# Performance work log

Hardware: AMD Instinct MI355X
Metric: run time of the kernel (lower is better)

Reference implementation:

```python
import jax, jax.numpy as jnp
import numpy as np

DIM = 256
NUM_HEADS = 4
HEAD_DIM = DIM // NUM_HEADS


def _linear_params(k, d_in, d_out):
    kw, kb = jax.random.split(k)
    lim = 1.0 / np.sqrt(d_in)
    W = jax.random.uniform(kw, (d_out, d_in), jnp.float32, -lim, lim)
    b = jax.random.uniform(kb, (d_out,), jnp.float32, -lim, lim)
    return W, b


def setup_inputs() -> dict:
    key = jax.random.key(0)
    ks = jax.random.split(key, 10)
    B, Nq, Nkv = 8, 4096, 256
    inp = {
        'node_emb': jax.random.normal(ks[0], (B, Nq, DIM), jnp.float32),
        'cluster_emb': jax.random.normal(ks[1], (B, Nkv, DIM), jnp.float32),
        'clustering_weights': jax.random.normal(ks[2], (B, Nq, Nkv), jnp.float32),
        'ln_q_g': jnp.ones((DIM,), jnp.float32), 'ln_q_b': jnp.zeros((DIM,), jnp.float32),
        'ln_kv_g': jnp.ones((DIM,), jnp.float32), 'ln_kv_b': jnp.zeros((DIM,), jnp.float32),
        'ln_out_g': jnp.ones((DIM,), jnp.float32), 'ln_out_b': jnp.zeros((DIM,), jnp.float32),
    }
    for name, k in [('q', ks[3]), ('k', ks[4]), ('v', ks[5]), ('o', ks[6])]:
        W, b = _linear_params(k, DIM, DIM)
        inp[f'W_{name}'], inp[f'b_{name}'] = W, b
    W1, b1 = _linear_params(ks[7], DIM, DIM)
    W2, b2 = _linear_params(ks[8], DIM, DIM)
    inp.update(W_m1=W1, b_m1=b1, W_m2=W2, b_m2=b2)
    return inp


def _layer_norm(x, g, b, eps=1e-5):
    mu = jnp.mean(x, axis=-1, keepdims=True)
    var = jnp.var(x, axis=-1, keepdims=True)
    return (x - mu) * jax.lax.rsqrt(var + eps) * g + b


def reference(node_emb, cluster_emb, clustering_weights,
              ln_q_g, ln_q_b, ln_kv_g, ln_kv_b, ln_out_g, ln_out_b,
              W_q, b_q, W_k, b_k, W_v, b_v, W_o, b_o,
              W_m1, b_m1, W_m2, b_m2):
    B, Nq, D = node_emb.shape
    Nkv = cluster_emb.shape[1]
    q_in = _layer_norm(node_emb, ln_q_g, ln_q_b)
    kv_in = _layer_norm(cluster_emb, ln_kv_g, ln_kv_b)
    # projections -> [B, H, N, hd]
    Q = (q_in @ W_q.T + b_q).reshape(B, Nq, NUM_HEADS, HEAD_DIM).transpose(0, 2, 1, 3)
    K = (kv_in @ W_k.T + b_k).reshape(B, Nkv, NUM_HEADS, HEAD_DIM).transpose(0, 2, 1, 3)
    V = (kv_in @ W_v.T + b_v).reshape(B, Nkv, NUM_HEADS, HEAD_DIM).transpose(0, 2, 1, 3)
    scores = jnp.einsum('bhqd,bhkd->bhqk', Q, K) / np.sqrt(HEAD_DIM)
    scores = scores + clustering_weights[:, None, :, :]
    attn = jax.nn.softmax(scores, axis=-1)
    ctx = jnp.einsum('bhqk,bhkd->bhqd', attn, V)
    ctx = ctx.transpose(0, 2, 1, 3).reshape(B, Nq, D)
    attn_out = ctx @ W_o.T + b_o
    x = node_emb + attn_out
    h = _layer_norm(x, ln_out_g, ln_out_b)
    h = jax.nn.gelu(h @ W_m1.T + b_m1, approximate=False) @ W_m2.T + b_m2
    out = x + h
    attn_matrix = attn.mean(axis=1)
    return out, attn_matrix
```

## Files before the change

### kernel.cpp

```cpp
#include <hip/hip_runtime.h>
#include <math.h>

typedef __attribute__((ext_vector_type(8))) short short8;
typedef __attribute__((ext_vector_type(4))) float f32x4;
typedef __attribute__((ext_vector_type(2))) unsigned int u32x2;

#define AS1 __attribute__((address_space(1)))
#define AS3 __attribute__((address_space(3)))

__device__ __forceinline__ float b2f(short s){
  return __uint_as_float(((unsigned int)(unsigned short)s) << 16);
}
__device__ __forceinline__ short f2b(float f){
  unsigned int u = __float_as_uint(f);
  u = (u + 0x7fffu + ((u >> 16) & 1u)) >> 16;
  return (short)u;
}
__device__ __forceinline__ unsigned pk2(float lo, float hi){
  return ((unsigned)(unsigned short)f2b(hi) << 16) | (unsigned)(unsigned short)f2b(lo);
}

__global__ __launch_bounds__(256) void cvt_w(
    const float* __restrict__ s0, const float* __restrict__ s1,
    const float* __restrict__ s2, const float* __restrict__ s3,
    const float* __restrict__ s4, const float* __restrict__ s5,
    short* __restrict__ dst)
{
  const float* srcs[6] = {s0, s1, s2, s3, s4, s5};
  int i = blockIdx.x * 256 + threadIdx.x;
  dst[i] = f2b(srcs[i >> 16][i & 65535]);
}

__global__ __launch_bounds__(256) void ln_k(
    const float* __restrict__ x, const float* __restrict__ g,
    const float* __restrict__ bta, short* __restrict__ y)
{
  const int row = blockIdx.x, t = threadIdx.x;
  const size_t base = (size_t)row * 256;
  float v = x[base + t];
  float s1 = v, s2 = v * v;
  #pragma unroll
  for (int off = 32; off; off >>= 1){ s1 += __shfl_down(s1, off); s2 += __shfl_down(s2, off); }
  __shared__ float a1[4], a2[4];
  __shared__ float mu_s, rs_s;
  if ((t & 63) == 0){ a1[t >> 6] = s1; a2[t >> 6] = s2; }
  __syncthreads();
  if (t == 0){
    float S1 = a1[0] + a1[1] + a1[2] + a1[3];
    float S2 = a2[0] + a2[1] + a2[2] + a2[3];
    float mu = S1 * 0.00390625f;
    float var = S2 * 0.00390625f - mu * mu;
    mu_s = mu; rs_s = rsqrtf(var + 1e-5f);
  }
  __syncthreads();
  y[base + t] = f2b((v - mu_s) * rs_s * g[t] + bta[t]);
}

template<int OT, int LNA>
__global__ __launch_bounds__(256, 2) void gemmW(
    const short* __restrict__ A, const float* __restrict__ Af,
    const short* __restrict__ W, const float* __restrict__ bias,
    short* __restrict__ outB,
    const float* __restrict__ lnag, const float* __restrict__ lnab)
{
  __shared__ short As[64][264];
  __shared__ short Ws[2][256][40];
  const int tid = threadIdx.x;
  const int m0 = blockIdx.x << 6;
  const int w = tid >> 6, lane = tid & 63;
  const int l15 = lane & 15, g = lane >> 4;

  if (LNA){
    const int row = tid >> 2, c0 = (tid & 3) << 6;
    float vv[64];
    const float* src = &Af[(size_t)(m0 + row) * 256 + c0];
    #pragma unroll
    for (int i = 0; i < 16; ++i) *(f32x4*)&vv[4 * i] = *(const f32x4*)&src[4 * i];
    float s1 = 0.f, s2 = 0.f;
    #pragma unroll
    for (int i = 0; i < 64; ++i){ s1 += vv[i]; s2 += vv[i] * vv[i]; }
    s1 += __shfl_xor(s1, 1); s2 += __shfl_xor(s2, 1);
    s1 += __shfl_xor(s1, 2); s2 += __shfl_xor(s2, 2);
    const float mu = s1 * 0.00390625f;
    const float rs = rsqrtf(s2 * 0.00390625f - mu * mu + 1e-5f);
    #pragma unroll
    for (int i = 0; i < 8; ++i){
      f32x4 gv0 = *(const f32x4*)&lnag[c0 + 8 * i];
      f32x4 gv1 = *(const f32x4*)&lnag[c0 + 8 * i + 4];
      f32x4 bv0 = *(const f32x4*)&lnab[c0 + 8 * i];
      f32x4 bv1 = *(const f32x4*)&lnab[c0 + 8 * i + 4];
      short8 o;
      #pragma unroll
      for (int j = 0; j < 4; ++j) o[j] = f2b((vv[8 * i + j] - mu) * rs * gv0[j] + bv0[j]);
      #pragma unroll
      for (int j = 0; j < 4; ++j) o[4 + j] = f2b((vv[8 * i + 4 + j] - mu) * rs * gv1[j] + bv1[j]);
      *(short8*)&As[row][c0 + 8 * i] = o;
    }
  } else {
    #pragma unroll
    for (int it = 0; it < 8; ++it){
      int idx = tid + (it << 8);
      int row = idx >> 5, c = (idx & 31) << 3;
      *(short8*)&As[row][c] = *(const short8*)&A[(size_t)(m0 + row) * 256 + c];
    }
  }
  #pragma unroll
  for (int it = 0; it < 4; ++it){
    int row = (it << 6) + (tid >> 2), c = (tid & 3) << 3;
    *(short8*)&Ws[0][row][c] = *(const short8*)&W[(size_t)row * 256 + c];
  }
  __syncthreads();

  f32x4 acc[16];
  #pragma unroll
  for (int nt = 0; nt < 16; ++nt) acc[nt] = {0.f, 0.f, 0.f, 0.f};

  int cur = 0;
  for (int s = 0; s < 8; ++s){
    const int k0 = s << 5;
    short8 wreg[4];
    if (s < 7){
      #pragma unroll
      for (int it = 0; it < 4; ++it)
        wreg[it] = *(const short8*)&W[(size_t)((it << 6) + (tid >> 2)) * 256 + k0 + 32 + ((tid & 3) << 3)];
    }
    short8 af = *(const short8*)&As[(w << 4) + l15][k0 + (g << 3)];
    #pragma unroll
    for (int nt = 0; nt < 16; ++nt){
      short8 bf = *(const short8*)&Ws[cur][(nt << 4) + l15][g << 3];
      acc[nt] = __builtin_amdgcn_mfma_f32_16x16x32_bf16(af, bf, acc[nt], 0, 0, 0);
    }
    if (s < 7){
      #pragma unroll
      for (int it = 0; it < 4; ++it)
        *(short8*)&Ws[cur ^ 1][(it << 6) + (tid >> 2)][(tid & 3) << 3] = wreg[it];
    }
    __syncthreads();
    cur ^= 1;
  }

  const int row_l = (w << 4) + (g << 2);
  #pragma unroll
  for (int nt = 0; nt < 16; ++nt){
    const int col = (nt << 4) + l15;
    const float bv = bias[col];
    #pragma unroll
    for (int r = 0; r < 4; ++r){
      const int m = m0 + row_l + r;
      float v = acc[nt][r] + bv;
      if (OT == 1){
        const int b_ = m >> 8, kvr = m & 255;
        const int knt = kvr >> 4, kl = kvr & 15;
        const int h = col >> 6, half = (col >> 5) & 1, kg = (col >> 3) & 3, kj = col & 7;
        outB[(((((size_t)(b_ * 4 + h) * 16 + knt) * 2 + half) * 4 + kg) * 16 + kl) * 8 + kj] = f2b(v);
      }
      if (OT == 2){
        const int b_ = m >> 8, kvj = m & 255;
        const int jp = (kvj & ~31) | (((kvj >> 2) & 3) << 3) | (((kvj >> 4) & 1) << 2) | (kvj & 3);
        const int h = col >> 6, dp = col & 63;
        const int kk = jp >> 5, vg = (jp >> 3) & 3, vj = jp & 7;
        const int vn2 = dp >> 4, vl = dp & 15;
        outB[(((((size_t)(b_ * 4 + h) * 8 + kk) * 4 + vn2) * 4 + vg) * 16 + vl) * 8 + vj] = f2b(v);
      }
      if (OT == 4){
        outB[((((size_t)blockIdx.x * 8 + (col >> 5)) * 4 + w) * 64
              + (((col >> 3) & 3) << 4) + (g << 2) + r) * 8 + (col & 7)] = f2b(v);
      }
    }
  }
}

__global__ __launch_bounds__(256, 2) void attn_k(
    const short* __restrict__ Qf, const short* __restrict__ Kf,
    const short* __restrict__ Vf, const float* __restrict__ cw,
    short* __restrict__ ctx, float* __restrict__ am_out)
{
  extern __shared__ __align__(16) short smem[];
  short* Kl = smem;
  short* Vl = smem + 16384;
  const int b = blockIdx.y;
  const int q0 = blockIdx.x << 6;
  const int tid = threadIdx.x;
  const int w = tid >> 6, lane = tid & 63;
  const int l15 = lane & 15, g = lane >> 4;
  const size_t qw = (size_t)b * 4096 + q0 + (w << 4);
  const size_t qblk = qw >> 4;
  const size_t tileQ = qblk >> 2;
  const int wQ = (int)(qblk & 3);
  const size_t tileC = (size_t)b * 64 + blockIdx.x;

#define STG(dst_, src_) do{ _Pragma("unroll")                                        \
  for (int it_ = 0; it_ < 8; ++it_){ int c_ = (it_ << 8) + tid;                      \
    __builtin_amdgcn_global_load_lds((const AS1 void*)((src_) + (c_ << 3)),          \
                                     (AS3 void*)((dst_) + (c_ << 3)), 16, 0, 0); } }while(0)

  unsigned cwp[16][2];
  f32x4 am[16];
  {
    char* reg = (char*)smem + (w << 13);
    #pragma unroll
    for (int j = 0; j < 16; ++j){
      f32x4 v = *(const f32x4*)&cw[(qw + j) * 256 + (lane << 2)];
      u32x2 d = { pk2(v[0], v[1]), pk2(v[2], v[3]) };
      unsigned off = ((j << 9) + (lane << 3)) ^ ((j & 7) << 4);
      *(u32x2*)(reg + off) = d;
    }
    __syncthreads();
    #pragma unroll
    for (int nt = 0; nt < 16; ++nt){
      unsigned base = ((l15 << 9) + (nt << 5) + (g << 3)) ^ ((l15 & 7) << 4);
      cwp[nt][0] = *(const unsigned*)(reg + base);
      cwp[nt][1] = *(const unsigned*)(reg + base + 4);
      am[nt] = {0.f, 0.f, 0.f, 0.f};
    }
    __syncthreads();
  }

  STG(Kl, Kf + ((size_t)(b * 4) << 14));
  __syncthreads();

  for (int h = 0; h < 4; ++h){
    STG(Vl, Vf + ((size_t)(b * 4 + h) << 14));
    short8 qf0 = *(const short8*)&Qf[(((tileQ * 8 + (h << 1)) * 4 + wQ) * 64 + lane) * 8];
    short8 qf1 = *(const short8*)&Qf[(((tileQ * 8 + (h << 1) + 1) * 4 + wQ) * 64 + lane) * 8];

    f32x4 acc[16];
    #pragma unroll
    for (int nt = 0; nt < 16; ++nt) acc[nt] = {0.f, 0.f, 0.f, 0.f};
    #pragma unroll
    for (int nt = 0; nt < 16; ++nt){
      short8 kf0 = *(const short8*)&Kl[(nt << 10) + (lane << 3)];
      acc[nt] = __builtin_amdgcn_mfma_f32_16x16x32_bf16(kf0, qf0, acc[nt], 0, 0, 0);
      short8 kf1 = *(const short8*)&Kl[(nt << 10) + 512 + (lane << 3)];
      acc[nt] = __builtin_amdgcn_mfma_f32_16x16x32_bf16(kf1, qf1, acc[nt], 0, 0, 0);
    }
    __syncthreads();
    if (h < 3) STG(Kl, Kf + ((size_t)(b * 4 + h + 1) << 14));

    float mx = -3.4e38f;
    #pragma unroll
    for (int nt = 0; nt < 16; ++nt){
      float c0 = __uint_as_float(cwp[nt][0] << 16);
      float c1 = __uint_as_float(cwp[nt][0] & 0xffff0000u);
      float c2 = __uint_as_float(cwp[nt][1] << 16);
      float c3 = __uint_as_float(cwp[nt][1] & 0xffff0000u);
      acc[nt][0] = acc[nt][0] * 0.125f + c0;
      acc[nt][1] = acc[nt][1] * 0.125f + c1;
      acc[nt][2] = acc[nt][2] * 0.125f + c2;
      acc[nt][3] = acc[nt][3] * 0.125f + c3;
      mx = fmaxf(mx, fmaxf(fmaxf(acc[nt][0], acc[nt][1]), fmaxf(acc[nt][2], acc[nt][3])));
    }
    mx = fmaxf(mx, __shfl_xor(mx, 16));
    mx = fmaxf(mx, __shfl_xor(mx, 32));
    float sm = 0.f;
    #pragma unroll
    for (int nt = 0; nt < 16; ++nt){
      #pragma unroll
      for (int r = 0; r < 4; ++r){
        float e = __expf(acc[nt][r] - mx);
        acc[nt][r] = e; sm += e;
      }
    }
    sm += __shfl_xor(sm, 16);
    sm += __shfl_xor(sm, 32);
    float inv = 1.f / sm;
    #pragma unroll
    for (int nt = 0; nt < 16; ++nt){
      #pragma unroll
      for (int r = 0; r < 4; ++r){
        float p = acc[nt][r] * inv;
        acc[nt][r] = p;
        am[nt][r] += 0.25f * p;
      }
    }
    f32x4 oc[4] = {{0,0,0,0},{0,0,0,0},{0,0,0,0},{0,0,0,0}};
    #pragma unroll
    for (int kk = 0; kk < 8; ++kk){
      union { short8 s; unsigned u[4]; } pa;
      pa.u[0] = pk2(acc[2 * kk][0],     acc[2 * kk][1]);
      pa.u[1] = pk2(acc[2 * kk][2],     acc[2 * kk][3]);
      pa.u[2] = pk2(acc[2 * kk + 1][0], acc[2 * kk + 1][1]);
      pa.u[3] = pk2(acc[2 * kk + 1][2], acc[2 * kk + 1][3]);
      #pragma unroll
      for (int n2 = 0; n2 < 4; ++n2){
        short8 vb = *(const short8*)&Vl[(((kk << 2) + n2) << 9) + (lane << 3)];
        oc[n2] = __builtin_amdgcn_mfma_f32_16x16x32_bf16(pa.s, vb, oc[n2], 0, 0, 0);
      }
    }
    #pragma unroll
    for (int n2 = 0; n2 < 4; ++n2){
      const int sctx = (h << 1) + (n2 >> 1);
      const int gctx = ((n2 & 1) << 1) + (l15 >> 3);
      const int j = l15 & 7;
      #pragma unroll
      for (int r = 0; r < 4; ++r)
        ctx[(((tileC * 8 + sctx) * 4 + w) * 64 + (gctx << 4) + (g << 2) + r) * 8 + j]
            = f2b(oc[n2][r]);
    }
    __syncthreads();
  }

  {
    char* reg = (char*)smem + (w << 14);
    #pragma unroll
    for (int nt = 0; nt < 16; ++nt){
      unsigned off = ((l15 << 10) + (nt << 6) + (g << 4)) ^ ((l15 & 7) << 4);
      *(f32x4*)(reg + off) = am[nt];
    }
    __syncthreads();
    #pragma unroll
    for (int i2 = 0; i2 < 16; ++i2){
      unsigned fb = (tid << 4) + (i2 << 12);
      unsigned rowin = (fb >> 10) & 15;
      f32x4 v = *(const f32x4*)((char*)smem + (fb ^ ((rowin & 7) << 4)));
      unsigned row = fb >> 10;
      *(f32x4*)&am_out[((size_t)b * 4096 + q0 + row) * 256 + ((fb & 1023) >> 2)] = v;
    }
  }
#undef STG
}

__global__ __launch_bounds__(256, 2) void tail_k(
    const short* __restrict__ ctxaf,
    const short* __restrict__ Wo, const short* __restrict__ Wm1,
    const short* __restrict__ Wm2,
    const float* __restrict__ b_o, const float* __restrict__ b_m1,
    const float* __restrict__ b_m2,
    const float* __restrict__ node,
    const float* __restrict__ lng, const float* __restrict__ lnb,
    float* __restrict__ outF)
{
  extern __shared__ __align__(16) short lds[];
  short (*As)[264] = (short(*)[264])lds;
  short (*Ws)[256][40] = (short(*)[256][40])(lds + 16896);
  const int tid = threadIdx.x;
  const int tile = blockIdx.x;
  const int m0 = tile << 6;
  const int w = tid >> 6, lane = tid & 63;
  const int l15 = lane & 15, g = lane >> 4;
  const int row_l = (w << 4) + (g << 2);

  short8 afr[8];
  f32x4 acc[16];

#define RUN_GEMM(WPTR, PROLOG_DONE)                                                  \
  do{                                                                                \
    if (!(PROLOG_DONE)){                                                             \
      short8 w0[4];                                                                  \
      _Pragma("unroll")                                                              \
      for (int it = 0; it < 4; ++it)                                                 \
        w0[it] = *(const short8*)&(WPTR)[(size_t)((it << 6) + (tid >> 2)) * 256 + ((tid & 3) << 3)]; \
      _Pragma("unroll")                                                              \
      for (int it = 0; it < 4; ++it)                                                 \
        *(short8*)&Ws[0][(it << 6) + (tid >> 2)][(tid & 3) << 3] = w0[it];           \
      __syncthreads();                                                               \
      _Pragma("unroll")                                                              \
      for (int s = 0; s < 8; ++s)                                                    \
        afr[s] = *(const short8*)&As[(w << 4) + l15][(s << 5) + (g << 3)];           \
    }                                                                                \
    _Pragma("unroll")                                                                \
    for (int nt = 0; nt < 16; ++nt) acc[nt] = (f32x4){0.f, 0.f, 0.f, 0.f};           \
    int cur = 0;                                                                     \
    for (int s = 0; s < 8; ++s){                                                     \
      const int k0 = s << 5;                                                         \
      short8 wreg[4];                                                                \
      if (s < 7){                                                                    \
        _Pragma("unroll")                                                            \
        for (int it = 0; it < 4; ++it)                                               \
          wreg[it] = *(const short8*)&(WPTR)[(size_t)((it << 6) + (tid >> 2)) * 256 + k0 + 32 + ((tid & 3) << 3)]; \
      }                                                                              \
      const short8 af = afr[s];                                                      \
      _Pragma("unroll")                                                              \
      for (int nt = 0; nt < 16; ++nt){                                               \
        short8 bf = *(const short8*)&Ws[cur][(nt << 4) + l15][g << 3];               \
        acc[nt] = __builtin_amdgcn_mfma_f32_16x16x32_bf16(af, bf, acc[nt], 0, 0, 0); \
      }                                                                              \
      if (s < 7){                                                                    \
        _Pragma("unroll")                                                            \
        for (int it = 0; it < 4; ++it)                                               \
          *(short8*)&Ws[cur ^ 1][(it << 6) + (tid >> 2)][(tid & 3) << 3] = wreg[it]; \
      }                                                                              \
      __syncthreads();                                                               \
      cur ^= 1;                                                                      \
    }                                                                                \
  }while(0)

  #pragma unroll
  for (int s = 0; s < 8; ++s)
    afr[s] = *(const short8*)&ctxaf[((((size_t)tile << 3) + s) * 4 + w) * 512 + (lane << 3)];
  {
    short8 w0[4];
    #pragma unroll
    for (int it = 0; it < 4; ++it)
      w0[it] = *(const short8*)&Wo[(size_t)((it << 6) + (tid >> 2)) * 256 + ((tid & 3) << 3)];
    #pragma unroll
    for (int it = 0; it < 4; ++it)
      *(short8*)&Ws[0][(it << 6) + (tid >> 2)][(tid & 3) << 3] = w0[it];
  }
  __syncthreads();
  RUN_GEMM(Wo, 1);

  f32x4 xv[16];
  #pragma unroll
  for (int nt = 0; nt < 16; ++nt){
    const int col = (nt << 4) + l15;
    const float bv = b_o[col];
    #pragma unroll
    for (int r = 0; r < 4; ++r)
      xv[nt][r] = acc[nt][r] + bv + node[(size_t)(m0 + row_l + r) * 256 + col];
  }
  #pragma unroll
  for (int r = 0; r < 4; ++r){
    float s1 = 0.f, s2 = 0.f;
    #pragma unroll
    for (int nt = 0; nt < 16; ++nt){ float v = xv[nt][r]; s1 += v; s2 += v * v; }
    #pragma unroll
    for (int off = 1; off < 16; off <<= 1){ s1 += __shfl_xor(s1, off); s2 += __shfl_xor(s2, off); }
    const float mu = s1 * 0.00390625f;
    const float rs = rsqrtf(s2 * 0.00390625f - mu * mu + 1e-5f);
    #pragma unroll
    for (int nt = 0; nt < 16; ++nt){
      const int col = (nt << 4) + l15;
      As[row_l + r][col] = f2b((xv[nt][r] - mu) * rs * lng[col] + lnb[col]);
    }
  }
  RUN_GEMM(Wm1, 0);
  #pragma unroll
  for (int nt = 0; nt < 16; ++nt){
    const int col = (nt << 4) + l15;
    const float bv = b_m1[col];
    #pragma unroll
    for (int r = 0; r < 4; ++r){
      float v = acc[nt][r] + bv;
      v = 0.5f * v * (1.0f + erff(v * 0.70710678118f));
      As[row_l + r][col] = f2b(v);
    }
  }
  RUN_GEMM(Wm2, 0);
  #pragma unroll
  for (int nt = 0; nt < 16; ++nt){
    const int col = (nt << 4) + l15;
    const float bv = b_m2[col];
    #pragma unroll
    for (int r = 0; r < 4; ++r)
      outF[(size_t)(m0 + row_l + r) * 256 + col] = acc[nt][r] + bv + xv[nt][r];
  }
#undef RUN_GEMM
}

extern "C" void kernel_launch(void* const* d_in, const int* in_sizes, int n_in,
                              void* d_out, int out_size, void* d_ws, size_t ws_size,
                              hipStream_t stream)
{
  const float* node_emb = (const float*)d_in[0];
  const float* cluster  = (const float*)d_in[1];
  const float* cw       = (const float*)d_in[2];
  const float* ln_q_g   = (const float*)d_in[3];
  const float* ln_q_b   = (const float*)d_in[4];
  const float* ln_kv_g  = (const float*)d_in[5];
  const float* ln_kv_b  = (const float*)d_in[6];
  const float* ln_o_g   = (const float*)d_in[7];
  const float* ln_o_b   = (const float*)d_in[8];
  const float* W_q  = (const float*)d_in[9];  const float* b_q  = (const float*)d_in[10];
  const float* W_k  = (const float*)d_in[11]; const float* b_k  = (const float*)d_in[12];
  const float* W_v  = (const float*)d_in[13]; const float* b_v  = (const float*)d_in[14];
  const float* W_o  = (const float*)d_in[15]; const float* b_o  = (const float*)d_in[16];
  const float* W_m1 = (const float*)d_in[17]; const float* b_m1 = (const float*)d_in[18];
  const float* W_m2 = (const float*)d_in[19]; const float* b_m2 = (const float*)d_in[20];

  char* ws = (char*)d_ws;
  short* Wbf   = (short*)ws;
  short* bufA  = (short*)(ws + 786432);
  short* bufB  = (short*)(ws + 786432 + 16777216);
  short* kvin  = (short*)(ws + 786432 + 2 * 16777216);
  short* kfrag = (short*)(ws + 786432 + 2 * 16777216 + 1048576);
  short* vfrag = (short*)(ws + 786432 + 2 * 16777216 + 2 * 1048576);

  float* outF = (float*)d_out;
  float* amof = (float*)d_out + 8388608;

  hipFuncSetAttribute((const void*)attn_k, hipFuncAttributeMaxDynamicSharedMemorySize, 65536);
  hipFuncSetAttribute((const void*)tail_k, hipFuncAttributeMaxDynamicSharedMemorySize, 74752);

  cvt_w<<<1536, 256, 0, stream>>>(W_q, W_k, W_v, W_o, W_m1, W_m2, Wbf);
  ln_k<<<2048, 256, 0, stream>>>(cluster, ln_kv_g, ln_kv_b, kvin);
  gemmW<4,1><<<512, 256, 0, stream>>>(nullptr, node_emb, Wbf, b_q, bufB, ln_q_g, ln_q_b);
  gemmW<1,0><<<32, 256, 0, stream>>>(kvin, nullptr, Wbf + 65536,  b_k, kfrag, nullptr, nullptr);
  gemmW<2,0><<<32, 256, 0, stream>>>(kvin, nullptr, Wbf + 131072, b_v, vfrag, nullptr, nullptr);
  attn_k<<<dim3(64, 8), 256, 65536, stream>>>(bufB, kfrag, vfrag, cw, bufA, amof);
  tail_k<<<512, 256, 74752, stream>>>(bufA, Wbf + 196608, Wbf + 262144, Wbf + 327680,
      b_o, b_m1, b_m2, node_emb, ln_o_g, ln_o_b, outF);
}
```

Baseline: 129.0 us.

## Stage tail-kernel weights via direct global-to-LDS loads from pre-tiled layout

```diff
diff --git a/kernel.cpp b/kernel.cpp
--- a/kernel.cpp
+++ b/kernel.cpp
@@ -19,16 +19,26 @@
 __device__ __forceinline__ unsigned pk2(float lo, float hi){
   return ((unsigned)(unsigned short)f2b(hi) << 16) | (unsigned)(unsigned short)f2b(lo);
 }
+__device__ __forceinline__ float ulo(unsigned u){ return __uint_as_float(u << 16); }
+__device__ __forceinline__ float uhi(unsigned u){ return __uint_as_float(u & 0xffff0000u); }
 
 __global__ __launch_bounds__(256) void cvt_w(
     const float* __restrict__ s0, const float* __restrict__ s1,
     const float* __restrict__ s2, const float* __restrict__ s3,
     const float* __restrict__ s4, const float* __restrict__ s5,
-    short* __restrict__ dst)
+    short* __restrict__ dst, short* __restrict__ dstS)
 {
   const float* srcs[6] = {s0, s1, s2, s3, s4, s5};
   int i = blockIdx.x * 256 + threadIdx.x;
-  dst[i] = f2b(srcs[i >> 16][i & 65535]);
+  int mat = i >> 16, rc = i & 65535;
+  short v = f2b(srcs[mat][rc]);
+  dst[i] = v;
+  if (mat >= 3){
+    int row = rc >> 8, col = rc & 255;
+    int d2 = (mat - 3) * 65536 + ((col >> 5) << 13) + (row << 5)
+           + (((col >> 3) & 3) << 3) + (col & 7);
+    dstS[d2] = v;
+  }
 }
 
 __global__ __launch_bounds__(256) void ln_k(
@@ -321,18 +331,15 @@
 }
 
 __global__ __launch_bounds__(256, 2) void tail_k(
-    const short* __restrict__ ctxaf,
-    const short* __restrict__ Wo, const short* __restrict__ Wm1,
-    const short* __restrict__ Wm2,
+    const short* __restrict__ ctxaf, const short* __restrict__ Wst,
     const float* __restrict__ b_o, const float* __restrict__ b_m1,
-    const float* __restrict__ b_m2,
-    const float* __restrict__ node,
+    const float* __restrict__ b_m2, const float* __restrict__ node,
     const float* __restrict__ lng, const float* __restrict__ lnb,
     float* __restrict__ outF)
 {
   extern __shared__ __align__(16) short lds[];
-  short (*As)[264] = (short(*)[264])lds;
-  short (*Ws)[256][40] = (short(*)[256][40])(lds + 16896);
+  short* Ws0 = lds + 16896;
+  short* Ws1 = Ws0 + 8192;
   const int tid = threadIdx.x;
   const int tile = blockIdx.x;
   const int m0 = tile << 6;
@@ -340,80 +347,63 @@
   const int l15 = lane & 15, g = lane >> 4;
   const int row_l = (w << 4) + (g << 2);
 
+#define ASW(row_, col_) (*(short*)((char*)lds + (row_) * 528 + ((((col_) << 1)) ^ (((row_) & 7) << 4))))
+#define ASR8(row_, boff_) (*(const short8*)((char*)lds + (row_) * 528 + ((boff_) ^ (((row_) & 7) << 4))))
+#define STGW(dst_, wmat_, s_) do{ _Pragma("unroll")                                  \
+  for (int it_ = 0; it_ < 4; ++it_){ int c_ = (it_ << 8) + tid;                      \
+    __builtin_amdgcn_global_load_lds(                                               \
+        (const AS1 void*)((wmat_) + ((size_t)(s_) << 13) + (c_ << 3)),              \
+        (AS3 void*)((dst_) + (c_ << 3)), 16, 0, 0); } }while(0)
+
+  f32x4 acc[16];
+
+  STGW(Ws0, Wst, 0);
   short8 afr[8];
-  f32x4 acc[16];
-
-#define RUN_GEMM(WPTR, PROLOG_DONE)                                                  \
-  do{                                                                                \
-    if (!(PROLOG_DONE)){                                                             \
-      short8 w0[4];                                                                  \
-      _Pragma("unroll")                                                              \
-      for (int it = 0; it < 4; ++it)                                                 \
-        w0[it] = *(const short8*)&(WPTR)[(size_t)((it << 6) + (tid >> 2)) * 256 + ((tid & 3) << 3)]; \
-      _Pragma("unroll")                                                              \
-      for (int it = 0; it < 4; ++it)                                                 \
-        *(short8*)&Ws[0][(it << 6) + (tid >> 2)][(tid & 3) << 3] = w0[it];           \
-      __syncthreads();                                                               \
-      _Pragma("unroll")                                                              \
-      for (int s = 0; s < 8; ++s)                                                    \
-        afr[s] = *(const short8*)&As[(w << 4) + l15][(s << 5) + (g << 3)];           \
-    }                                                                                \
-    _Pragma("unroll")                                                                \
-    for (int nt = 0; nt < 16; ++nt) acc[nt] = (f32x4){0.f, 0.f, 0.f, 0.f};           \
-    int cur = 0;                                                                     \
-    for (int s = 0; s < 8; ++s){                                                     \
-      const int k0 = s << 5;                                                         \
-      short8 wreg[4];                                                                \
-      if (s < 7){                                                                    \
-        _Pragma("unroll")                                                            \
-        for (int it = 0; it < 4; ++it)                                               \
-          wreg[it] = *(const short8*)&(WPTR)[(size_t)((it << 6) + (tid >> 2)) * 256 + k0 + 32 + ((tid & 3) << 3)]; \
-      }                                                                              \
-      const short8 af = afr[s];                                                      \
-      _Pragma("unroll")                                                              \
-      for (int nt = 0; nt < 16; ++nt){                                               \
-        short8 bf = *(const short8*)&Ws[cur][(nt << 4) + l15][g << 3];               \
-        acc[nt] = __builtin_amdgcn_mfma_f32_16x16x32_bf16(af, bf, acc[nt], 0, 0, 0); \
-      }                                                                              \
-      if (s < 7){                                                                    \
-        _Pragma("unroll")                                                            \
-        for (int it = 0; it < 4; ++it)                                               \
-          *(short8*)&Ws[cur ^ 1][(it << 6) + (tid >> 2)][(tid & 3) << 3] = wreg[it]; \
-      }                                                                              \
-      __syncthreads();                                                               \
-      cur ^= 1;                                                                      \
-    }                                                                                \
-  }while(0)
-
   #pragma unroll
   for (int s = 0; s < 8; ++s)
     afr[s] = *(const short8*)&ctxaf[((((size_t)tile << 3) + s) * 4 + w) * 512 + (lane << 3)];
+  __syncthreads();
+  #pragma unroll
+  for (int nt = 0; nt < 16; ++nt) acc[nt] = {0.f, 0.f, 0.f, 0.f};
   {
-    short8 w0[4];
-    #pragma unroll
-    for (int it = 0; it < 4; ++it)
-      w0[it] = *(const short8*)&Wo[(size_t)((it << 6) + (tid >> 2)) * 256 + ((tid & 3) << 3)];
-    #pragma unroll
-    for (int it = 0; it < 4; ++it)
-      *(short8*)&Ws[0][(it << 6) + (tid >> 2)][(tid & 3) << 3] = w0[it];
-  }
-  __syncthreads();
-  RUN_GEMM(Wo, 1);
-
-  f32x4 xv[16];
+    int cur = 0;
+    #pragma unroll
+    for (int s = 0; s < 8; ++s){
+      short* rbuf = cur ? Ws1 : Ws0;
+      short* sbuf = cur ? Ws0 : Ws1;
+      if (s < 7) STGW(sbuf, Wst, s + 1);
+      const short8 af = afr[s];
+      #pragma unroll
+      for (int nt = 0; nt < 16; ++nt){
+        short8 bf = *(const short8*)&rbuf[((nt << 4) + l15) * 32 + (g << 3)];
+        acc[nt] = __builtin_amdgcn_mfma_f32_16x16x32_bf16(af, bf, acc[nt], 0, 0, 0);
+      }
+      __syncthreads();
+      cur ^= 1;
+    }
+  }
+
+  unsigned xvp[16][2];
   #pragma unroll
   for (int nt = 0; nt < 16; ++nt){
     const int col = (nt << 4) + l15;
     const float bv = b_o[col];
-    #pragma unroll
-    for (int r = 0; r < 4; ++r)
-      xv[nt][r] = acc[nt][r] + bv + node[(size_t)(m0 + row_l + r) * 256 + col];
+    float x0 = acc[nt][0] + bv + node[(size_t)(m0 + row_l + 0) * 256 + col];
+    float x1 = acc[nt][1] + bv + node[(size_t)(m0 + row_l + 1) * 256 + col];
+    float x2 = acc[nt][2] + bv + node[(size_t)(m0 + row_l + 2) * 256 + col];
+    float x3 = acc[nt][3] + bv + node[(size_t)(m0 + row_l + 3) * 256 + col];
+    xvp[nt][0] = pk2(x0, x1);
+    xvp[nt][1] = pk2(x2, x3);
   }
   #pragma unroll
   for (int r = 0; r < 4; ++r){
     float s1 = 0.f, s2 = 0.f;
     #pragma unroll
-    for (int nt = 0; nt < 16; ++nt){ float v = xv[nt][r]; s1 += v; s2 += v * v; }
+    for (int nt = 0; nt < 16; ++nt){
+      float v = (r == 0) ? ulo(xvp[nt][0]) : (r == 1) ? uhi(xvp[nt][0])
+              : (r == 2) ? ulo(xvp[nt][1]) : uhi(xvp[nt][1]);
+      s1 += v; s2 += v * v;
+    }
     #pragma unroll
     for (int off = 1; off < 16; off <<= 1){ s1 += __shfl_xor(s1, off); s2 += __shfl_xor(s2, off); }
     const float mu = s1 * 0.00390625f;
@@ -421,10 +411,34 @@
     #pragma unroll
     for (int nt = 0; nt < 16; ++nt){
       const int col = (nt << 4) + l15;
-      As[row_l + r][col] = f2b((xv[nt][r] - mu) * rs * lng[col] + lnb[col]);
-    }
-  }
-  RUN_GEMM(Wm1, 0);
+      float v = (r == 0) ? ulo(xvp[nt][0]) : (r == 1) ? uhi(xvp[nt][0])
+              : (r == 2) ? ulo(xvp[nt][1]) : uhi(xvp[nt][1]);
+      ASW(row_l + r, col) = f2b((v - mu) * rs * lng[col] + lnb[col]);
+    }
+  }
+
+  {
+    const short* Wm1 = Wst + 65536;
+    STGW(Ws0, Wm1, 0);
+    __syncthreads();
+    #pragma unroll
+    for (int nt = 0; nt < 16; ++nt) acc[nt] = {0.f, 0.f, 0.f, 0.f};
+    int cur = 0;
+    #pragma unroll
+    for (int s = 0; s < 8; ++s){
+      short* rbuf = cur ? Ws1 : Ws0;
+      short* sbuf = cur ? Ws0 : Ws1;
+      if (s < 7) STGW(sbuf, Wm1, s + 1);
+      const short8 af = ASR8((w << 4) + l15, (s << 6) + (g << 4));
+      #pragma unroll
+      for (int nt = 0; nt < 16; ++nt){
+        short8 bf = *(const short8*)&rbuf[((nt << 4) + l15) * 32 + (g << 3)];
+        acc[nt] = __builtin_amdgcn_mfma_f32_16x16x32_bf16(af, bf, acc[nt], 0, 0, 0);
+      }
+      __syncthreads();
+      cur ^= 1;
+    }
+  }
   #pragma unroll
   for (int nt = 0; nt < 16; ++nt){
     const int col = (nt << 4) + l15;
@@ -433,19 +447,46 @@
     for (int r = 0; r < 4; ++r){
       float v = acc[nt][r] + bv;
       v = 0.5f * v * (1.0f + erff(v * 0.70710678118f));
-      As[row_l + r][col] = f2b(v);
-    }
-  }
-  RUN_GEMM(Wm2, 0);
+      ASW(row_l + r, col) = f2b(v);
+    }
+  }
+
+  {
+    const short* Wm2 = Wst + 131072;
+    STGW(Ws0, Wm2, 0);
+    __syncthreads();
+    #pragma unroll
+    for (int nt = 0; nt < 16; ++nt) acc[nt] = {0.f, 0.f, 0.f, 0.f};
+    int cur = 0;
+    #pragma unroll
+    for (int s = 0; s < 8; ++s){
+      short* rbuf = cur ? Ws1 : Ws0;
+      short* sbuf = cur ? Ws0 : Ws1;
+      if (s < 7) STGW(sbuf, Wm2, s + 1);
+      const short8 af = ASR8((w << 4) + l15, (s << 6) + (g << 4));
+      #pragma unroll
+      for (int nt = 0; nt < 16; ++nt){
+        short8 bf = *(const short8*)&rbuf[((nt << 4) + l15) * 32 + (g << 3)];
+        acc[nt] = __builtin_amdgcn_mfma_f32_16x16x32_bf16(af, bf, acc[nt], 0, 0, 0);
+      }
+      __syncthreads();
+      cur ^= 1;
+    }
+  }
   #pragma unroll
   for (int nt = 0; nt < 16; ++nt){
     const int col = (nt << 4) + l15;
     const float bv = b_m2[col];
     #pragma unroll
-    for (int r = 0; r < 4; ++r)
-      outF[(size_t)(m0 + row_l + r) * 256 + col] = acc[nt][r] + bv + xv[nt][r];
-  }
-#undef RUN_GEMM
+    for (int r = 0; r < 4; ++r){
+      float xr = (r == 0) ? ulo(xvp[nt][0]) : (r == 1) ? uhi(xvp[nt][0])
+               : (r == 2) ? ulo(xvp[nt][1]) : uhi(xvp[nt][1]);
+      outF[(size_t)(m0 + row_l + r) * 256 + col] = acc[nt][r] + bv + xr;
+    }
+  }
+#undef ASW
+#undef ASR8
+#undef STGW
 }
 
 extern "C" void kernel_launch(void* const* d_in, const int* in_sizes, int n_in,
@@ -470,24 +511,25 @@
 
   char* ws = (char*)d_ws;
   short* Wbf   = (short*)ws;
-  short* bufA  = (short*)(ws + 786432);
-  short* bufB  = (short*)(ws + 786432 + 16777216);
-  short* kvin  = (short*)(ws + 786432 + 2 * 16777216);
-  short* kfrag = (short*)(ws + 786432 + 2 * 16777216 + 1048576);
-  short* vfrag = (short*)(ws + 786432 + 2 * 16777216 + 2 * 1048576);
+  short* Wst   = (short*)(ws + 786432);
+  short* bufA  = (short*)(ws + 1179648);
+  short* bufB  = (short*)(ws + 1179648 + 16777216);
+  short* kvin  = (short*)(ws + 1179648 + 2 * 16777216);
+  short* kfrag = (short*)(ws + 1179648 + 2 * 16777216 + 1048576);
+  short* vfrag = (short*)(ws + 1179648 + 2 * 16777216 + 2 * 1048576);
 
   float* outF = (float*)d_out;
   float* amof = (float*)d_out + 8388608;
 
   hipFuncSetAttribute((const void*)attn_k, hipFuncAttributeMaxDynamicSharedMemorySize, 65536);
-  hipFuncSetAttribute((const void*)tail_k, hipFuncAttributeMaxDynamicSharedMemorySize, 74752);
-
-  cvt_w<<<1536, 256, 0, stream>>>(W_q, W_k, W_v, W_o, W_m1, W_m2, Wbf);
+  hipFuncSetAttribute((const void*)tail_k, hipFuncAttributeMaxDynamicSharedMemorySize, 66560);
+
+  cvt_w<<<1536, 256, 0, stream>>>(W_q, W_k, W_v, W_o, W_m1, W_m2, Wbf, Wst);
   ln_k<<<2048, 256, 0, stream>>>(cluster, ln_kv_g, ln_kv_b, kvin);
   gemmW<4,1><<<512, 256, 0, stream>>>(nullptr, node_emb, Wbf, b_q, bufB, ln_q_g, ln_q_b);
   gemmW<1,0><<<32, 256, 0, stream>>>(kvin, nullptr, Wbf + 65536,  b_k, kfrag, nullptr, nullptr);
   gemmW<2,0><<<32, 256, 0, stream>>>(kvin, nullptr, Wbf + 131072, b_v, vfrag, nullptr, nullptr);
   attn_k<<<dim3(64, 8), 256, 65536, stream>>>(bufB, kfrag, vfrag, cw, bufA, amof);
-  tail_k<<<512, 256, 74752, stream>>>(bufA, Wbf + 196608, Wbf + 262144, Wbf + 327680,
-      b_o, b_m1, b_m2, node_emb, ln_o_g, ln_o_b, outF);
-}
+  tail_k<<<512, 256, 66560, stream>>>(bufA, Wst, b_o, b_m1, b_m2,
+      node_emb, ln_o_g, ln_o_b, outF);
+}
```

Result: faster. 123.5 us (-4.3%).
